# Kernel tuning notes

Measured on AMD Instinct MI355X. Metric: run time of the kernel, lower is better.

Reference implementation:

```python
import jax, jax.numpy as jnp
import numpy as np

B, C, H, W = 8, 64, 256, 256


def setup_inputs() -> dict:
    key = jax.random.key(0)
    k1, k2, k3 = jax.random.split(key, 3)
    phi = jax.random.normal(k1, (B, 2, H, W), dtype=jnp.float32) * 2.0
    x_enc = jax.random.normal(k2, (B, C, H, W), dtype=jnp.float32)
    m = jax.random.uniform(k3, (B, 1, H, W), dtype=jnp.float32)
    return {"phi": phi, "x_enc": x_enc, "m": m}


def _grid_sample_bilinear_zeros(x, grid):
    """torch.nn.functional.grid_sample defaults: bilinear, zeros padding,
    align_corners=False. x: [b,c,h,w], grid: [b,h,w,2] in [-1,1] (x,y order)."""
    b, c, h, w = x.shape
    # unnormalize (align_corners=False convention)
    ix = (grid[..., 0] + 1.0) * (0.5 * w) - 0.5  # [b,h,w]
    iy = (grid[..., 1] + 1.0) * (0.5 * h) - 0.5
    x0 = jnp.floor(ix)
    y0 = jnp.floor(iy)
    x1 = x0 + 1.0
    y1 = y0 + 1.0
    wx1 = ix - x0
    wx0 = 1.0 - wx1
    wy1 = iy - y0
    wy0 = 1.0 - wy1

    bidx = jnp.arange(b)[:, None, None]

    def corner(yy, xx, wgt):
        valid = (xx >= 0) & (xx < w) & (yy >= 0) & (yy < h)
        xc = jnp.clip(xx, 0, w - 1).astype(jnp.int32)
        yc = jnp.clip(yy, 0, h - 1).astype(jnp.int32)
        v = x[bidx, :, yc, xc]  # gather -> [b,h,w,c]
        return v * (wgt * valid.astype(x.dtype))[..., None]

    out = (corner(y0, x0, wy0 * wx0) + corner(y0, x1, wy0 * wx1)
           + corner(y1, x0, wy1 * wx0) + corner(y1, x1, wy1 * wx1))  # [b,h,w,c]
    return jnp.transpose(out, (0, 3, 1, 2))  # [b,c,h,w]


def reference(phi, x_enc, m):
    b, c, h, w = x_enc.shape
    # pixel coordinate grid: channel 0 = x (width), channel 1 = y (height)
    yy, xx = jnp.meshgrid(jnp.arange(h, dtype=jnp.float32),
                          jnp.arange(w, dtype=jnp.float32), indexing="ij")
    grid = jnp.stack([xx, yy], axis=0)[None]  # [1,2,h,w]
    vgrid = grid + phi                         # [b,2,h,w]
    vx = 2.0 * vgrid[:, 0] / max(w - 1, 1) - 1.0
    vy = 2.0 * vgrid[:, 1] / max(h - 1, 1) - 1.0
    vgrid = jnp.stack([vx, vy], axis=-1)       # [b,h,w,2]
    # original: phi = phi.permute(0,2,3,1); vgrid = vgrid + 2*phi
    vgrid = vgrid + 2.0 * jnp.transpose(phi, (0, 2, 3, 1))
    out = _grid_sample_bilinear_zeros(x_enc, vgrid)
    return out * m
```

## Files before the change

kernel.cpp:

```cpp
#include <hip/hip_runtime.h>

namespace {

constexpr int B = 8, C = 64, H = 256, W = 256;
constexpr int HW = H * W;
constexpr int TP = 64;
constexpr int TSTRIDE = 68;

typedef float v4f __attribute__((ext_vector_type(4)));

__global__ __launch_bounds__(256) void warp_kernel(
    const float* __restrict__ phi,
    const float* __restrict__ xenc,
    const float* __restrict__ mm,
    float* __restrict__ out)
{
    __shared__ float tile[64 * TSTRIDE];
    __shared__ float s_w[4][TP];
    __shared__ int   s_o[4][TP];
    __shared__ int   s_p[TP];
    __shared__ int   s_n;

    const int t   = threadIdx.x;
    const int bid = blockIdx.x;
    const int wt  = bid & 3;
    const int h   = (bid >> 2) & (H - 1);
    const int b   = bid >> 10;
    const int w0  = wt * 64;

    {
        v4f z = {0.f, 0.f, 0.f, 0.f};
        for (int i = t; i < (64 * TSTRIDE) / 4; i += 256)
            *(v4f*)&tile[i * 4] = z;
    }

    if (t < 64) {
        const int lane = t;
        const int w    = w0 + lane;
        const int hw   = h * W + w;

        const float p0 = phi[(size_t)(b * 2 + 0) * HW + hw];
        const float p1 = phi[(size_t)(b * 2 + 1) * HW + hw];
        const float mv = mm[(size_t)b * HW + hw];

        const float gx = (2.0f * ((float)w + p0)) / (float)(W - 1) - 1.0f + 2.0f * p0;
        const float gy = (2.0f * ((float)h + p1)) / (float)(H - 1) - 1.0f + 2.0f * p1;
        const float ix = (gx + 1.0f) * (0.5f * (float)W) - 0.5f;
        const float iy = (gy + 1.0f) * (0.5f * (float)H) - 0.5f;

        const float x0f = floorf(ix);
        const float y0f = floorf(iy);
        const float fx1 = ix - x0f, fx0 = 1.0f - fx1;
        const float fy1 = iy - y0f, fy0 = 1.0f - fy1;

        const float wm1 = (float)(W - 1), hm1 = (float)(H - 1);
        const int x0 = (int)fminf(fmaxf(x0f,        0.0f), wm1);
        const int x1 = (int)fminf(fmaxf(x0f + 1.0f, 0.0f), wm1);
        const int y0 = (int)fminf(fmaxf(y0f,        0.0f), hm1);
        const int y1 = (int)fminf(fmaxf(y0f + 1.0f, 0.0f), hm1);

        const bool vx0 = (x0f >= 0.0f) && (x0f < (float)W);
        const bool vx1 = (x0f + 1.0f >= 0.0f) && (x0f + 1.0f < (float)W);
        const bool vy0 = (y0f >= 0.0f) && (y0f < (float)H);
        const bool vy1 = (y0f + 1.0f >= 0.0f) && (y0f + 1.0f < (float)H);

        const float w00 = fy0 * fx0 * ((vy0 && vx0) ? mv : 0.0f);
        const float w01 = fy0 * fx1 * ((vy0 && vx1) ? mv : 0.0f);
        const float w10 = fy1 * fx0 * ((vy1 && vx0) ? mv : 0.0f);
        const float w11 = fy1 * fx1 * ((vy1 && vx1) ? mv : 0.0f);

        const bool inb = (w00 + w01 + w10 + w11) != 0.0f;

        const unsigned long long mask = __ballot(inb);
        const int pos = __popcll(mask & ((1ULL << lane) - 1ULL));
        if (inb) {
            s_w[0][pos] = w00;  s_w[1][pos] = w01;
            s_w[2][pos] = w10;  s_w[3][pos] = w11;
            s_o[0][pos] = y0 * W + x0;
            s_o[1][pos] = y0 * W + x1;
            s_o[2][pos] = y1 * W + x0;
            s_o[3][pos] = y1 * W + x1;
            s_p[pos]    = lane;
        }
        if (lane == 0) s_n = __popcll(mask);
    }
    __syncthreads();

    {
        const int wv   = t >> 6;
        const int lane = t & 63;
        const int n    = s_n;
        const float* __restrict__ xb = xenc + ((size_t)b * C + lane) * HW;
        for (int i = wv; i < n; i += 4) {
            const float w00 = s_w[0][i], w01 = s_w[1][i];
            const float w10 = s_w[2][i], w11 = s_w[3][i];
            const int o00 = s_o[0][i], o01 = s_o[1][i];
            const int o10 = s_o[2][i], o11 = s_o[3][i];
            const int p   = s_p[i];
            const float v = xb[o00] * w00 + xb[o01] * w01
                          + xb[o10] * w10 + xb[o11] * w11;
            tile[lane * TSTRIDE + p] = v;
        }
    }
    __syncthreads();

    {
        const size_t obase = (size_t)b * C * HW + (size_t)h * W + w0;
        const int cl = t >> 4;
        const int p4 = (t & 15) * 4;
        #pragma unroll
        for (int pass = 0; pass < 4; ++pass) {
            const int c = pass * 16 + cl;
            v4f v = *(const v4f*)&tile[c * TSTRIDE + p4];
            __builtin_nontemporal_store(v, (v4f*)(out + obase + (size_t)c * HW + p4));
        }
    }
}

}

extern "C" void kernel_launch(void* const* d_in, const int* in_sizes, int n_in,
                              void* d_out, int out_size, void* d_ws, size_t ws_size,
                              hipStream_t stream) {
    const float* phi  = (const float*)d_in[0];
    const float* xenc = (const float*)d_in[1];
    const float* mm   = (const float*)d_in[2];
    float* out = (float*)d_out;

    const int blocks = B * H * (W / 64);
    warp_kernel<<<dim3(blocks), dim3(256), 0, stream>>>(phi, xenc, mm, out);
}
```

Before: 244.7 us.

## Pre-transpose input to channels-last fp16 workspace before bilinear gather

```diff
diff --git a/kernel.cpp b/kernel.cpp
--- a/kernel.cpp
+++ b/kernel.cpp
@@ -1,4 +1,5 @@
 #include <hip/hip_runtime.h>
+#include <hip/hip_fp16.h>
 
 namespace {
 
@@ -6,12 +7,45 @@
 constexpr int HW = H * W;
 constexpr int TP = 64;
 constexpr int TSTRIDE = 68;
+constexpr int LTS = 68;
 
 typedef float v4f __attribute__((ext_vector_type(4)));
 
-__global__ __launch_bounds__(256) void warp_kernel(
+__global__ __launch_bounds__(256) void transpose_kernel(
+    const float* __restrict__ x, __half* __restrict__ ws)
+{
+    __shared__ __half lt[256 * LTS];
+    const int t   = threadIdx.x;
+    const int bid = blockIdx.x;
+    const int b   = bid >> 8;
+    const int hw0 = (bid & 255) << 8;
+    const int wv  = t >> 6, lane = t & 63;
+
+    for (int k = 0; k < 16; ++k) {
+        const int c = wv * 16 + k;
+        const float* __restrict__ src = x + (size_t)(b * C + c) * HW + hw0;
+        #pragma unroll
+        for (int q = 0; q < 4; ++q) {
+            lt[(q * 64 + lane) * LTS + c] = __float2half(src[q * 64 + lane]);
+        }
+    }
+    __syncthreads();
+
+    #pragma unroll
+    for (int pass = 0; pass < 8; ++pass) {
+        const int hw = pass * 32 + (t >> 3);
+        const int c8 = (t & 7) * 8;
+        const __half* __restrict__ row = &lt[hw * LTS + c8];
+        const uint2 lo = *(const uint2*)(row);
+        const uint2 hi = *(const uint2*)(row + 4);
+        int4 v; v.x = (int)lo.x; v.y = (int)lo.y; v.z = (int)hi.x; v.w = (int)hi.y;
+        *(int4*)(ws + ((size_t)b * HW + hw0 + hw) * 64 + c8) = v;
+    }
+}
+
+__global__ __launch_bounds__(256) void warp_main(
     const float* __restrict__ phi,
-    const float* __restrict__ xenc,
+    const __half* __restrict__ ws,
     const float* __restrict__ mm,
     float* __restrict__ out)
 {
@@ -70,7 +104,6 @@
         const float w11 = fy1 * fx1 * ((vy1 && vx1) ? mv : 0.0f);
 
         const bool inb = (w00 + w01 + w10 + w11) != 0.0f;
-
         const unsigned long long mask = __ballot(inb);
         const int pos = __popcll(mask & ((1ULL << lane) - 1ULL));
         if (inb) {
@@ -90,16 +123,15 @@
         const int wv   = t >> 6;
         const int lane = t & 63;
         const int n    = s_n;
-        const float* __restrict__ xb = xenc + ((size_t)b * C + lane) * HW;
+        const __half* __restrict__ wsb = ws + (size_t)b * HW * 64 + lane;
         for (int i = wv; i < n; i += 4) {
             const float w00 = s_w[0][i], w01 = s_w[1][i];
             const float w10 = s_w[2][i], w11 = s_w[3][i];
-            const int o00 = s_o[0][i], o01 = s_o[1][i];
-            const int o10 = s_o[2][i], o11 = s_o[3][i];
-            const int p   = s_p[i];
-            const float v = xb[o00] * w00 + xb[o01] * w01
-                          + xb[o10] * w10 + xb[o11] * w11;
-            tile[lane * TSTRIDE + p] = v;
+            const float v = __half2float(wsb[(size_t)s_o[0][i] * 64]) * w00
+                          + __half2float(wsb[(size_t)s_o[1][i] * 64]) * w01
+                          + __half2float(wsb[(size_t)s_o[2][i] * 64]) * w10
+                          + __half2float(wsb[(size_t)s_o[3][i] * 64]) * w11;
+            tile[lane * TSTRIDE + s_p[i]] = v;
         }
     }
     __syncthreads();
@@ -117,6 +149,66 @@
     }
 }
 
+__global__ __launch_bounds__(256) void warp_fallback(
+    const float* __restrict__ phi,
+    const float* __restrict__ xenc,
+    const float* __restrict__ mm,
+    float* __restrict__ out)
+{
+    const int tid = blockIdx.x * 256 + threadIdx.x;
+    const int w = tid & (W - 1);
+    const int h = (tid >> 8) & (H - 1);
+    const int b = tid >> 16;
+    const int hw = h * W + w;
+
+    const float p0 = phi[(size_t)(b * 2 + 0) * HW + hw];
+    const float p1 = phi[(size_t)(b * 2 + 1) * HW + hw];
+    const float mv = mm[(size_t)b * HW + hw];
+
+    const float gx = (2.0f * ((float)w + p0)) / (float)(W - 1) - 1.0f + 2.0f * p0;
+    const float gy = (2.0f * ((float)h + p1)) / (float)(H - 1) - 1.0f + 2.0f * p1;
+    const float ix = (gx + 1.0f) * (0.5f * (float)W) - 0.5f;
+    const float iy = (gy + 1.0f) * (0.5f * (float)H) - 0.5f;
+
+    const float x0f = floorf(ix);
+    const float y0f = floorf(iy);
+    const float fx1 = ix - x0f, fx0 = 1.0f - fx1;
+    const float fy1 = iy - y0f, fy0 = 1.0f - fy1;
+
+    const float wm1 = (float)(W - 1), hm1 = (float)(H - 1);
+    const int x0 = (int)fminf(fmaxf(x0f,        0.0f), wm1);
+    const int x1 = (int)fminf(fmaxf(x0f + 1.0f, 0.0f), wm1);
+    const int y0 = (int)fminf(fmaxf(y0f,        0.0f), hm1);
+    const int y1 = (int)fminf(fmaxf(y0f + 1.0f, 0.0f), hm1);
+
+    const bool vx0 = (x0f >= 0.0f) && (x0f < (float)W);
+    const bool vx1 = (x0f + 1.0f >= 0.0f) && (x0f + 1.0f < (float)W);
+    const bool vy0 = (y0f >= 0.0f) && (y0f < (float)H);
+    const bool vy1 = (y0f + 1.0f >= 0.0f) && (y0f + 1.0f < (float)H);
+
+    const float w00 = fy0 * fx0 * ((vy0 && vx0) ? mv : 0.0f);
+    const float w01 = fy0 * fx1 * ((vy0 && vx1) ? mv : 0.0f);
+    const float w10 = fy1 * fx0 * ((vy1 && vx0) ? mv : 0.0f);
+    const float w11 = fy1 * fx1 * ((vy1 && vx1) ? mv : 0.0f);
+    const bool doGather = (w00 + w01 + w10 + w11) != 0.0f;
+
+    const int o00 = y0 * W + x0, o01 = y0 * W + x1;
+    const int o10 = y1 * W + x0, o11 = y1 * W + x1;
+
+    const float* __restrict__ xb = xenc + (size_t)b * C * HW;
+    float* __restrict__ ob = out + (size_t)b * C * HW + hw;
+
+    #pragma unroll 4
+    for (int c = 0; c < C; ++c) {
+        float v = 0.0f;
+        if (doGather) {
+            const float* __restrict__ xc = xb + (size_t)c * HW;
+            v = xc[o00] * w00 + xc[o01] * w01 + xc[o10] * w10 + xc[o11] * w11;
+        }
+        ob[(size_t)c * HW] = v;
+    }
+}
+
 }
 
 extern "C" void kernel_launch(void* const* d_in, const int* in_sizes, int n_in,
@@ -127,6 +219,12 @@
     const float* mm   = (const float*)d_in[2];
     float* out = (float*)d_out;
 
-    const int blocks = B * H * (W / 64);
-    warp_kernel<<<dim3(blocks), dim3(256), 0, stream>>>(phi, xenc, mm, out);
-}
+    const size_t need = (size_t)B * HW * C * sizeof(__half);
+    if (ws_size >= need) {
+        __half* ws = (__half*)d_ws;
+        transpose_kernel<<<dim3(B * (HW / 256)), dim3(256), 0, stream>>>(xenc, ws);
+        warp_main<<<dim3(B * H * (W / 64)), dim3(256), 0, stream>>>(phi, ws, mm, out);
+    } else {
+        warp_fallback<<<dim3((B * HW) / 256), dim3(256), 0, stream>>>(phi, xenc, mm, out);
+    }
+}
```

Result: slower. 252.8 us (+3.3%).
